# Kernel optimization log

Measured on AMD Instinct MI355X. Metric: run time of the kernel, lower is better.

Reference implementation:

```python
import jax, jax.numpy as jnp
import numpy as np

ALPHA = 0.2  # LeakyReLU negative slope (init alpha)


def setup_inputs() -> dict:
    key = jax.random.key(0)
    k1, k2, k3, k4 = jax.random.split(key, 4)
    B, N, D = 32, 1024, 64
    H, E = 4, 16  # n_heads, out_features per head
    return {
        "input": jax.random.normal(k1, (B, N, D), dtype=jnp.float32),
        "adj": jax.random.uniform(k2, (N, N), dtype=jnp.float32),  # unused by the module
        "W": jax.random.normal(k3, (H, D, E), dtype=jnp.float32) * 0.1,
        "a": jax.random.normal(k4, (2 * E, 1), dtype=jnp.float32) * 0.1,
    }


def reference(input, adj, W, a):
    # h: [B, H, N, E]
    h = jnp.einsum('bnd,hde->bhne', input, W)
    E = h.shape[-1]
    # Original concatenates [h_j, h_i] along features then dots with a,
    # i.e. e[b,h,i,j] = leakyrelu(a[:E]\cdot h_j + a[E:]\cdot h_i).
    a_dst = a[:E, 0]   # applied to the softmax (j) axis
    a_src = a[E:, 0]   # applied to the query (i) axis
    s_src = jnp.einsum('bhne,e->bhn', h, a_src)  # [B,H,N]
    s_dst = jnp.einsum('bhne,e->bhn', h, a_dst)  # [B,H,N]
    e = jax.nn.leaky_relu(s_src[..., :, None] + s_dst[..., None, :],
                          negative_slope=ALPHA)  # [B,H,N,N]
    attention = jax.nn.softmax(e, axis=-1)  # dropout skipped (eval mode)
    h_prime = jnp.einsum('bhij,bhje->bhie', attention, h)  # [B,H,N,E]
    B, H, N, _ = h_prime.shape
    # Faithful to torch: .view(B, N, -1) on a [B,H,N,E] contiguous tensor
    # is a raw row-major reshape (no transpose), reproduced exactly here.
    return h_prime.reshape(B, N, H * E)
```

## Files before the change

### kernel.cpp

```cpp
#include <hip/hip_runtime.h>

typedef _Float16 f16;
typedef f16 f16x8 __attribute__((ext_vector_type(8)));
typedef float f32x4 __attribute__((ext_vector_type(4)));

constexpr int Bc = 32, Nc = 1024, Dc = 64, Hc = 4, Ec = 16;
constexpr int HPL = 1032;

__global__ __launch_bounds__(256) void gat_proj2(const float* __restrict__ input,
                                                 const float* __restrict__ W,
                                                 const float* __restrict__ a,
                                                 f16* __restrict__ h16t,
                                                 float* __restrict__ s_src,
                                                 float* __restrict__ s_dst) {
    __shared__ float W_lds[Dc * Ec];
    __shared__ float a_lds[2 * Ec];
    __shared__ alignas(16) f16 T[Ec][136];

    const int tid  = threadIdx.x;
    const int blk  = blockIdx.x;
    const int bh   = blk >> 3;
    const int hh   = bh & (Hc - 1);
    const int b    = bh >> 2;
    const int n0   = (blk & 7) * 128;
    const int half = tid & 1;
    const int nl   = tid >> 1;
    const int n    = n0 + nl;

    ((float4*)W_lds)[tid] = ((const float4*)(W + hh * Dc * Ec))[tid];
    if (tid < 2 * Ec) a_lds[tid] = a[tid];
    __syncthreads();

    const float4* in_row = (const float4*)(input + ((size_t)b * Nc + n) * Dc);

    float acc[8];
#pragma unroll
    for (int e = 0; e < 8; ++e) acc[e] = 0.f;

#pragma unroll
    for (int d4 = 0; d4 < Dc / 4; ++d4) {
        float4 x = in_row[d4];
        float xs[4] = {x.x, x.y, x.z, x.w};
#pragma unroll
        for (int k = 0; k < 4; ++k) {
            const float xv = xs[k];
            const float* wrow = &W_lds[(d4 * 4 + k) * Ec + half * 8];
#pragma unroll
            for (int e = 0; e < 8; ++e) acc[e] = fmaf(xv, wrow[e], acc[e]);
        }
    }

    {
        float sd = 0.f, ss = 0.f;
#pragma unroll
        for (int e = 0; e < 8; ++e) {
            sd = fmaf(acc[e], a_lds[half * 8 + e],      sd);
            ss = fmaf(acc[e], a_lds[16 + half * 8 + e], ss);
        }
        sd += __shfl_xor(sd, 1, 64);
        ss += __shfl_xor(ss, 1, 64);
        if (half == 0) {
            s_dst[bh * Nc + n] = sd;
            s_src[bh * Nc + n] = ss;
        }
    }

#pragma unroll
    for (int e = 0; e < 8; ++e) T[half * 8 + e][nl] = (f16)acc[e];
    __syncthreads();

    {
        const int e2 = tid >> 4;
        const int ch = tid & 15;
        *(float4*)(h16t + (size_t)bh * Ec * Nc + (size_t)e2 * Nc + n0 + ch * 8) =
            *(const float4*)(&T[e2][ch * 8]);
    }
}

__global__ __launch_bounds__(512) void gat_attn10(const f16* __restrict__ h16t,
                                                  const float* __restrict__ s_src,
                                                  const float* __restrict__ s_dst,
                                                  float* __restrict__ out) {
    __shared__ alignas(16) f16 hv_t[Ec * HPL];
    __shared__ alignas(16) f16 w_lds[Nc];
    __shared__ alignas(16) f16 v_lds[Nc];
    __shared__ float red[8];

    const int bh    = blockIdx.x;
    const int ihalf = blockIdx.y;
    const int tid   = threadIdx.x;
    const int lane  = tid & 63;
    const int wave  = tid >> 6;
    const int row   = lane & 15;
    const int quad  = lane >> 4;

    f16x8 h8[4];
    {
        const float4* src = (const float4*)(h16t + (size_t)bh * Ec * Nc);
#pragma unroll
        for (int cc = 0; cc < 4; ++cc) {
            float4 t = src[cc * 512 + tid];
            h8[cc] = *(f16x8*)&t;
        }
    }

    const float sd0 = s_dst[bh * Nc + tid];
    const float sd1 = s_dst[bh * Nc + 512 + tid];
    {
        float m = fmaxf(sd0, sd1);
#pragma unroll
        for (int off = 1; off < 64; off <<= 1) m = fmaxf(m, __shfl_xor(m, off, 64));
        if (lane == 0) red[wave] = m;
    }
    __syncthreads();
    float maxd = red[0];
#pragma unroll
    for (int w = 1; w < 8; ++w) maxd = fmaxf(maxd, red[w]);

    w_lds[tid]       = (f16)__expf(0.8f * (sd0 - maxd));
    w_lds[512 + tid] = (f16)__expf(0.8f * (sd1 - maxd));
    v_lds[tid]       = (f16)__expf(0.2f * (sd0 - maxd));
    v_lds[512 + tid] = (f16)__expf(0.2f * (sd1 - maxd));

    const int ibase = ihalf * 512 + wave * 64;
    f16x8 C8[4];
#pragma unroll
    for (int it = 0; it < 4; ++it) {
        const float si = s_src[bh * Nc + ibase + it * 16 + row];
        const float c1 = si + maxd;
        const float Cf = (c1 >= 0.f) ? __expf(-0.8f * c1) : 1.0f;
        const f16 ch = (f16)Cf;
        C8[it] = (f16x8){ch, ch, ch, ch, ch, ch, ch, ch};
    }
    __syncthreads();

    {
        float4* dst = (float4*)hv_t;
#pragma unroll
        for (int cc = 0; cc < 4; ++cc) {
            const int c  = cc * 512 + tid;
            const int e  = c >> 7;
            const int jc = c & 127;
            const f16x8 v8 = *(const f16x8*)(&v_lds[jc * 8]);
            f16x8 hv = h8[cc] * v8;
            dst[e * 129 + jc] = *(float4*)&hv;
        }
    }
    __syncthreads();

    f32x4 accN[4] = {};
    f32x4 accD[4] = {};

    const f16* wp = w_lds + quad * 8;
    const f16* vp = v_lds + quad * 8;
    const f16* bp = hv_t + row * HPL + quad * 8;

#pragma unroll 4
    for (int kt = 0; kt < 32; ++kt) {
        const f16x8 w8  = *(const f16x8*)(wp + kt * 32);
        const f16x8 v8  = *(const f16x8*)(vp + kt * 32);
        const f16x8 hv8 = *(const f16x8*)(bp + kt * 32);
#pragma unroll
        for (int it = 0; it < 4; ++it) {
            const f16x8 pm = __builtin_elementwise_max(w8, C8[it]);
            accN[it] = __builtin_amdgcn_mfma_f32_16x16x32_f16(pm, hv8, accN[it], 0, 0, 0);
            accD[it] = __builtin_amdgcn_mfma_f32_16x16x32_f16(pm, v8,  accD[it], 0, 0, 0);
        }
    }

#pragma unroll
    for (int it = 0; it < 4; ++it) {
#pragma unroll
        for (int r = 0; r < 4; ++r) {
            const float inv = __builtin_amdgcn_rcpf(accD[it][r]);
            const int i = ibase + it * 16 + quad * 4 + r;
            out[((size_t)(bh * Nc + i)) * Ec + row] = accN[it][r] * inv;
        }
    }
}

extern "C" void kernel_launch(void* const* d_in, const int* in_sizes, int n_in,
                              void* d_out, int out_size, void* d_ws, size_t ws_size,
                              hipStream_t stream) {
    const float* input = (const float*)d_in[0];
    const float* W = (const float*)d_in[2];
    const float* a = (const float*)d_in[3];
    float* out = (float*)d_out;

    char* ws = (char*)d_ws;
    f16*   h16t  = (f16*)(ws);
    float* s_src = (float*)(ws + 4194304);
    float* s_dst = (float*)(ws + 4194304 + 524288);

    gat_proj2<<<dim3(1024), dim3(256), 0, stream>>>(input, W, a, h16t, s_src, s_dst);
    gat_attn10<<<dim3(Bc * Hc, 2), dim3(512), 0, stream>>>(h16t, s_src, s_dst, out);
}
```

Before: 23.87 us.

## Split attention K-loop across two wave groups with LDS partial reduction

Doubles the attention block to 1024 threads. The two halves of the waves each process half of the j (key) dimension, and their partial numerator and denominator accumulators are combined through shared memory that reuses the hv_t buffer. The aim is more waves per CU to hide MFMA and LDS latency and to shorten each wave's serial K loop. In exchange it adds two extra barriers, an LDS reduction step, and higher register pressure under the 1024-thread launch bound.

```diff
diff --git a/kernel.cpp b/kernel.cpp
--- a/kernel.cpp
+++ b/kernel.cpp
@@ -77,37 +77,41 @@
     }
 }
 
-__global__ __launch_bounds__(512) void gat_attn10(const f16* __restrict__ h16t,
-                                                  const float* __restrict__ s_src,
-                                                  const float* __restrict__ s_dst,
-                                                  float* __restrict__ out) {
-    __shared__ alignas(16) f16 hv_t[Ec * HPL];
-    __shared__ alignas(16) f16 w_lds[Nc];
-    __shared__ alignas(16) f16 v_lds[Nc];
-    __shared__ float red[8];
+__global__ __launch_bounds__(1024) void gat_attn11(const f16* __restrict__ h16t,
+                                                   const float* __restrict__ s_src,
+                                                   const float* __restrict__ s_dst,
+                                                   float* __restrict__ out) {
+    __shared__ alignas(16) char smem[33024 + 2048 + 2048 + 64];
+    f16* hv_t  = (f16*)smem;
+    f16* w_lds = (f16*)(smem + 33024);
+    f16* v_lds = (f16*)(smem + 35072);
+    float* red = (float*)(smem + 37120);
+    float* pN  = (float*)smem;
+    float* pD  = (float*)(smem + 33024);
 
     const int bh    = blockIdx.x;
     const int ihalf = blockIdx.y;
     const int tid   = threadIdx.x;
     const int lane  = tid & 63;
     const int wave  = tid >> 6;
+    const int wgrp  = wave & 7;
+    const int khalf = wave >> 3;
     const int row   = lane & 15;
     const int quad  = lane >> 4;
 
-    f16x8 h8[4];
+    f16x8 h8[2];
     {
         const float4* src = (const float4*)(h16t + (size_t)bh * Ec * Nc);
 #pragma unroll
-        for (int cc = 0; cc < 4; ++cc) {
-            float4 t = src[cc * 512 + tid];
+        for (int cc = 0; cc < 2; ++cc) {
+            float4 t = src[cc * 1024 + tid];
             h8[cc] = *(f16x8*)&t;
         }
     }
 
     const float sd0 = s_dst[bh * Nc + tid];
-    const float sd1 = s_dst[bh * Nc + 512 + tid];
-    {
-        float m = fmaxf(sd0, sd1);
+    {
+        float m = sd0;
 #pragma unroll
         for (int off = 1; off < 64; off <<= 1) m = fmaxf(m, __shfl_xor(m, off, 64));
         if (lane == 0) red[wave] = m;
@@ -115,14 +119,12 @@
     __syncthreads();
     float maxd = red[0];
 #pragma unroll
-    for (int w = 1; w < 8; ++w) maxd = fmaxf(maxd, red[w]);
-
-    w_lds[tid]       = (f16)__expf(0.8f * (sd0 - maxd));
-    w_lds[512 + tid] = (f16)__expf(0.8f * (sd1 - maxd));
-    v_lds[tid]       = (f16)__expf(0.2f * (sd0 - maxd));
-    v_lds[512 + tid] = (f16)__expf(0.2f * (sd1 - maxd));
-
-    const int ibase = ihalf * 512 + wave * 64;
+    for (int w = 1; w < 16; ++w) maxd = fmaxf(maxd, red[w]);
+
+    w_lds[tid] = (f16)__expf(0.8f * (sd0 - maxd));
+    v_lds[tid] = (f16)__expf(0.2f * (sd0 - maxd));
+
+    const int ibase = ihalf * 512 + wgrp * 64;
     f16x8 C8[4];
 #pragma unroll
     for (int it = 0; it < 4; ++it) {
@@ -137,8 +139,8 @@
     {
         float4* dst = (float4*)hv_t;
 #pragma unroll
-        for (int cc = 0; cc < 4; ++cc) {
-            const int c  = cc * 512 + tid;
+        for (int cc = 0; cc < 2; ++cc) {
+            const int c  = cc * 1024 + tid;
             const int e  = c >> 7;
             const int jc = c & 127;
             const f16x8 v8 = *(const f16x8*)(&v_lds[jc * 8]);
@@ -151,12 +153,12 @@
     f32x4 accN[4] = {};
     f32x4 accD[4] = {};
 
-    const f16* wp = w_lds + quad * 8;
-    const f16* vp = v_lds + quad * 8;
-    const f16* bp = hv_t + row * HPL + quad * 8;
+    const f16* wp = w_lds + quad * 8 + khalf * 512;
+    const f16* vp = v_lds + quad * 8 + khalf * 512;
+    const f16* bp = hv_t + row * HPL + quad * 8 + khalf * 512;
 
 #pragma unroll 4
-    for (int kt = 0; kt < 32; ++kt) {
+    for (int kt = 0; kt < 16; ++kt) {
         const f16x8 w8  = *(const f16x8*)(wp + kt * 32);
         const f16x8 v8  = *(const f16x8*)(vp + kt * 32);
         const f16x8 hv8 = *(const f16x8*)(bp + kt * 32);
@@ -168,13 +170,33 @@
         }
     }
 
-#pragma unroll
-    for (int it = 0; it < 4; ++it) {
-#pragma unroll
-        for (int r = 0; r < 4; ++r) {
-            const float inv = __builtin_amdgcn_rcpf(accD[it][r]);
-            const int i = ibase + it * 16 + quad * 4 + r;
-            out[((size_t)(bh * Nc + i)) * Ec + row] = accN[it][r] * inv;
+    __syncthreads();
+
+    if (khalf == 1) {
+#pragma unroll
+        for (int it = 0; it < 4; ++it) {
+#pragma unroll
+            for (int r = 0; r < 4; ++r) {
+                pN[(((wgrp * 4 + it) * 4 + r) * 4 + quad) * 16 + row] = accN[it][r];
+                if (row == 0) pD[((wgrp * 4 + it) * 4 + r) * 4 + quad] = accD[it][r];
+            }
+        }
+    }
+    __syncthreads();
+
+    if (khalf == 0) {
+#pragma unroll
+        for (int it = 0; it < 4; ++it) {
+#pragma unroll
+            for (int r = 0; r < 4; ++r) {
+                const float nsum = accN[it][r] +
+                    pN[(((wgrp * 4 + it) * 4 + r) * 4 + quad) * 16 + row];
+                const float dsum = accD[it][r] +
+                    pD[((wgrp * 4 + it) * 4 + r) * 4 + quad];
+                const float inv = __builtin_amdgcn_rcpf(dsum);
+                const int i = ibase + it * 16 + quad * 4 + r;
+                out[((size_t)(bh * Nc + i)) * Ec + row] = nsum * inv;
+            }
         }
     }
 }
@@ -193,5 +215,5 @@
     float* s_dst = (float*)(ws + 4194304 + 524288);
 
     gat_proj2<<<dim3(1024), dim3(256), 0, stream>>>(input, W, a, h16t, s_src, s_dst);
-    gat_attn10<<<dim3(Bc * Hc, 2), dim3(512), 0, stream>>>(h16t, s_src, s_dst, out);
+    gat_attn11<<<dim3(Bc * Hc, 2), dim3(1024), 0, stream>>>(h16t, s_src, s_dst, out);
 }
```

Result: slower. 24.87 us (+4.2%).

## Compute projection with MFMA and derive attention scores from precombined W·a

Applied to the files above, without the earlier changes.

The projection kernel now computes h = x·W with 16x16x32 f16 MFMA instructions instead of scalar FMA loops over W in LDS. The attention scores s_src and s_dst are computed separately in fp32 as x·(W·a), with W·a folded into two 64-vectors per block. The aim is to cut ALU work in the projection stage. In exchange it adds a second read of the input rows, strided scalar global loads for W and x, and f16 rounding of the inputs before the matmul.

```diff
diff --git a/kernel.cpp b/kernel.cpp
--- a/kernel.cpp
+++ b/kernel.cpp
@@ -1,20 +1,20 @@
 #include <hip/hip_runtime.h>
 
 typedef _Float16 f16;
+typedef f16 f16x4 __attribute__((ext_vector_type(4)));
 typedef f16 f16x8 __attribute__((ext_vector_type(8)));
 typedef float f32x4 __attribute__((ext_vector_type(4)));
 
 constexpr int Bc = 32, Nc = 1024, Dc = 64, Hc = 4, Ec = 16;
 constexpr int HPL = 1032;
 
-__global__ __launch_bounds__(256) void gat_proj2(const float* __restrict__ input,
-                                                 const float* __restrict__ W,
-                                                 const float* __restrict__ a,
-                                                 f16* __restrict__ h16t,
-                                                 float* __restrict__ s_src,
-                                                 float* __restrict__ s_dst) {
-    __shared__ float W_lds[Dc * Ec];
-    __shared__ float a_lds[2 * Ec];
+__global__ __launch_bounds__(256) void gat_projm2(const float* __restrict__ input,
+                                                  const float* __restrict__ W,
+                                                  const float* __restrict__ a,
+                                                  f16* __restrict__ h16t,
+                                                  float* __restrict__ s_src,
+                                                  float* __restrict__ s_dst) {
+    __shared__ float wa_lds[2][Dc];
     __shared__ alignas(16) f16 T[Ec][136];
 
     const int tid  = threadIdx.x;
@@ -23,50 +23,49 @@
     const int hh   = bh & (Hc - 1);
     const int b    = bh >> 2;
     const int n0   = (blk & 7) * 128;
-    const int half = tid & 1;
-    const int nl   = tid >> 1;
-    const int n    = n0 + nl;
-
-    ((float4*)W_lds)[tid] = ((const float4*)(W + hh * Dc * Ec))[tid];
-    if (tid < 2 * Ec) a_lds[tid] = a[tid];
-    __syncthreads();
-
-    const float4* in_row = (const float4*)(input + ((size_t)b * Nc + n) * Dc);
-
-    float acc[8];
-#pragma unroll
-    for (int e = 0; e < 8; ++e) acc[e] = 0.f;
-
-#pragma unroll
-    for (int d4 = 0; d4 < Dc / 4; ++d4) {
-        float4 x = in_row[d4];
-        float xs[4] = {x.x, x.y, x.z, x.w};
-#pragma unroll
-        for (int k = 0; k < 4; ++k) {
-            const float xv = xs[k];
-            const float* wrow = &W_lds[(d4 * 4 + k) * Ec + half * 8];
-#pragma unroll
-            for (int e = 0; e < 8; ++e) acc[e] = fmaf(xv, wrow[e], acc[e]);
-        }
-    }
-
-    {
-        float sd = 0.f, ss = 0.f;
-#pragma unroll
-        for (int e = 0; e < 8; ++e) {
-            sd = fmaf(acc[e], a_lds[half * 8 + e],      sd);
-            ss = fmaf(acc[e], a_lds[16 + half * 8 + e], ss);
-        }
-        sd += __shfl_xor(sd, 1, 64);
-        ss += __shfl_xor(ss, 1, 64);
-        if (half == 0) {
-            s_dst[bh * Nc + n] = sd;
-            s_src[bh * Nc + n] = ss;
-        }
-    }
-
-#pragma unroll
-    for (int e = 0; e < 8; ++e) T[half * 8 + e][nl] = (f16)acc[e];
+    const int lane = tid & 63;
+    const int wave = tid >> 6;
+    const int row  = lane & 15;
+    const int quad = lane >> 4;
+
+    if (tid < 2 * Dc) {
+        const int d = tid & (Dc - 1), which = tid >> 6;
+        const float* wr = W + hh * Dc * Ec + d * Ec;
+        const float* av = a + which * Ec;
+        float acc = 0.f;
+#pragma unroll
+        for (int e = 0; e < Ec; ++e) acc = fmaf(wr[e], av[e], acc);
+        wa_lds[which][d] = acc;
+    }
+
+    f16x8 bW0, bW1;
+    {
+        const float* wp = W + hh * Dc * Ec + row;
+#pragma unroll
+        for (int j = 0; j < 8; ++j) {
+            bW0[j] = (f16)wp[(quad * 8 + j) * Ec];
+            bW1[j] = (f16)wp[(32 + quad * 8 + j) * Ec];
+        }
+    }
+
+#pragma unroll
+    for (int t = 0; t < 2; ++t) {
+        const int nl = wave * 32 + t * 16;
+        const float* ip = input + ((size_t)b * Nc + n0 + nl + row) * Dc;
+        f16x8 x0, x1;
+#pragma unroll
+        for (int j = 0; j < 8; ++j) {
+            x0[j] = (f16)ip[quad * 8 + j];
+            x1[j] = (f16)ip[32 + quad * 8 + j];
+        }
+        f32x4 hD = {};
+        hD = __builtin_amdgcn_mfma_f32_16x16x32_f16(x0, bW0, hD, 0, 0, 0);
+        hD = __builtin_amdgcn_mfma_f32_16x16x32_f16(x1, bW1, hD, 0, 0, 0);
+        f16x4 hp;
+#pragma unroll
+        for (int r = 0; r < 4; ++r) hp[r] = (f16)hD[r];
+        *(f16x4*)(&T[row][nl + quad * 4]) = hp;
+    }
     __syncthreads();
 
     {
@@ -74,6 +73,27 @@
         const int ch = tid & 15;
         *(float4*)(h16t + (size_t)bh * Ec * Nc + (size_t)e2 * Nc + n0 + ch * 8) =
             *(const float4*)(&T[e2][ch * 8]);
+    }
+
+    {
+        const int nl = tid >> 1;
+        const int dh = (tid & 1) * 8;
+        const float4* xr  = (const float4*)(input + ((size_t)b * Nc + n0 + nl) * Dc) + dh;
+        const float4* wdp = (const float4*)wa_lds[0] + dh;
+        const float4* wsp = (const float4*)wa_lds[1] + dh;
+        float sd = 0.f, ss = 0.f;
+#pragma unroll
+        for (int d4 = 0; d4 < 8; ++d4) {
+            float4 x = xr[d4], wd = wdp[d4], wsx = wsp[d4];
+            sd = fmaf(x.x, wd.x,  fmaf(x.y, wd.y,  fmaf(x.z, wd.z,  fmaf(x.w, wd.w,  sd))));
+            ss = fmaf(x.x, wsx.x, fmaf(x.y, wsx.y, fmaf(x.z, wsx.z, fmaf(x.w, wsx.w, ss))));
+        }
+        sd += __shfl_xor(sd, 1, 64);
+        ss += __shfl_xor(ss, 1, 64);
+        if ((tid & 1) == 0) {
+            s_dst[bh * Nc + n0 + nl] = sd;
+            s_src[bh * Nc + n0 + nl] = ss;
+        }
     }
 }
 
@@ -192,6 +212,6 @@
     float* s_src = (float*)(ws + 4194304);
     float* s_dst = (float*)(ws + 4194304 + 524288);
 
-    gat_proj2<<<dim3(1024), dim3(256), 0, stream>>>(input, W, a, h16t, s_src, s_dst);
+    gat_projm2<<<dim3(1024), dim3(256), 0, stream>>>(input, W, a, h16t, s_src, s_dst);
     gat_attn10<<<dim3(Bc * Hc, 2), dim3(512), 0, stream>>>(h16t, s_src, s_dst, out);
 }
```

Measured after the change: 25.98 us. 8.8% more time.
